# Performance work log

Measured on AMD Instinct MI355X. Metric: run time of the kernel, lower is better.

The kernel has to match this reference:

```python
import jax, jax.numpy as jnp
import numpy as np

EPS = 1e-5

def _bn(x, gamma, beta):
    # BatchNorm with track_running_stats=False: batch stats over all dims but last
    axes = tuple(range(x.ndim - 1))
    mu = jnp.mean(x, axis=axes)
    var = jnp.var(x, axis=axes)  # biased, as torch uses for normalization
    return (x - mu) * jax.lax.rsqrt(var + EPS) * gamma + beta

def setup_inputs() -> dict:
    B, N, D = 8, 200, 128
    key = jax.random.key(0)
    ks = jax.random.split(key, 14)
    s = 1.0 / np.sqrt(D)
    def w(k):
        return jax.random.uniform(k, (D, D), jnp.float32, -s, s)
    def b(k):
        return jax.random.uniform(k, (D,), jnp.float32, -s, s)
    return {
        'h': jax.random.normal(ks[0], (B, N, D), jnp.float32),
        'e': jax.random.normal(ks[1], (B, N, N, D), jnp.float32),
        'Uw': w(ks[2]), 'Ub': b(ks[3]),
        'Vw': w(ks[4]), 'Vb': b(ks[5]),
        'Aw': w(ks[6]), 'Ab': b(ks[7]),
        'Bw': w(ks[8]), 'Bb': b(ks[9]),
        'Cw': w(ks[10]), 'Cb': b(ks[11]),
        'gamma_h': jnp.ones((D,), jnp.float32), 'beta_h': jnp.zeros((D,), jnp.float32),
        'gamma_e': jnp.ones((D,), jnp.float32), 'beta_e': jnp.zeros((D,), jnp.float32),
    }

def reference(h, e, Uw, Ub, Vw, Vb, Aw, Ab, Bw, Bb, Cw, Cb,
              gamma_h, beta_h, gamma_e, beta_e):
    h_in, e_in = h, e
    Uh = h @ Uw.T + Ub                      # [B,N,D]
    Vh = h @ Vw.T + Vb                      # [B,N,D]
    Ah = h @ Aw.T + Ab
    Bh = h @ Bw.T + Bb
    Ce = e @ Cw.T + Cb                      # [B,N,N,D]
    # e_new[b,i,j,d] = Ah[b,j,d] + Bh[b,i,d] + Ce[b,i,j,d]
    e_new = Ah[:, None, :, :] + Bh[:, :, None, :] + Ce
    gates = jax.nn.sigmoid(e_new)           # [B,N,N,D]
    # sum aggregation over source nodes j with Vh broadcast over i
    agg = jnp.sum(gates * Vh[:, None, :, :], axis=2)  # [B,N,D]
    h_new = Uh + agg
    h_out = h_in + jax.nn.relu(_bn(h_new, gamma_h, beta_h))
    e_out = e_in + jax.nn.relu(_bn(e_new, gamma_e, beta_e))
    return (h_out, e_out)
```

## Files before the change

kernel.cpp:

```cpp
#include <hip/hip_runtime.h>
#include <hip/hip_bf16.h>


#define B_ 8
#define N_ 200
#define D_ 128
#define BN_ (B_*N_)
#define HN_ (BN_*D_)

typedef __attribute__((ext_vector_type(8))) short short8v;
typedef __attribute__((ext_vector_type(4))) short short4v;
typedef __attribute__((ext_vector_type(4))) float float4v;
typedef __attribute__((ext_vector_type(4))) unsigned int uint4v;

__device__ __forceinline__ unsigned short f2b(float f) {
  unsigned u = __float_as_uint(f);
  u += 0x7FFFu + ((u >> 16) & 1u);
  return (unsigned short)(u >> 16);
}

__global__ __launch_bounds__(256) void prelin_kernel(
    const float* __restrict__ h,
    const float* __restrict__ Uw, const float* __restrict__ Ub,
    const float* __restrict__ Vw, const float* __restrict__ Vb,
    const float* __restrict__ Aw, const float* __restrict__ Ab,
    const float* __restrict__ Bw, const float* __restrict__ Bb,
    const float* __restrict__ Cw,
    float* __restrict__ Uh, float* __restrict__ Vh,
    float* __restrict__ Ah, float* __restrict__ Bh,
    unsigned short* __restrict__ Cwbf) {
  const int tid = threadIdx.x;
  if (blockIdx.x >= 100) {
    int g = (blockIdx.x - 100) * 1024 + tid * 4;
    float4v v = *(const float4v*)(Cw + g);
    short4v s;
    s.x = (short)f2b(v.x); s.y = (short)f2b(v.y);
    s.z = (short)f2b(v.z); s.w = (short)f2b(v.w);
    *(short4v*)(Cwbf + g) = s;
    return;
  }
  const int r0 = blockIdx.x * 16;
  __shared__ float hs[16][128];
  for (int k = 0; k < 2; k++) {
    int g = k * 256 + tid;
    int row = g >> 5, col4 = g & 31;
    *(float4v*)&hs[row][col4 * 4] =
        *(const float4v*)(h + (size_t)(r0 + row) * D_ + col4 * 4);
  }
  __syncthreads();
  const int c0 = tid, c1 = tid + 256;
  const float* w0 = (c0 < 128) ? (Uw + c0 * 128) : (Vw + (c0 - 128) * 128);
  const float  b0 = (c0 < 128) ? Ub[c0] : Vb[c0 - 128];
  const float* w1 = (c1 < 384) ? (Aw + (c1 - 256) * 128) : (Bw + (c1 - 384) * 128);
  const float  b1 = (c1 < 384) ? Ab[c1 - 256] : Bb[c1 - 384];
  float acc0[16], acc1[16];
#pragma unroll
  for (int r = 0; r < 16; r++) { acc0[r] = 0.f; acc1[r] = 0.f; }
  for (int k = 0; k < 128; k += 4) {
    float4v w0v = *(const float4v*)(w0 + k);
    float4v w1v = *(const float4v*)(w1 + k);
#pragma unroll
    for (int r = 0; r < 16; r++) {
      float4v hv = *(const float4v*)&hs[r][k];
      acc0[r] = fmaf(hv.x, w0v.x, fmaf(hv.y, w0v.y, fmaf(hv.z, w0v.z, fmaf(hv.w, w0v.w, acc0[r]))));
      acc1[r] = fmaf(hv.x, w1v.x, fmaf(hv.y, w1v.y, fmaf(hv.z, w1v.z, fmaf(hv.w, w1v.w, acc1[r]))));
    }
  }
  float* dst0 = (c0 < 128) ? Uh : Vh; const int cc0 = c0 & 127;
  float* dst1 = (c1 < 384) ? Ah : Bh; const int cc1 = (c1 - 256) & 127;
#pragma unroll
  for (int r = 0; r < 16; r++) {
    dst0[(size_t)(r0 + r) * D_ + cc0] = acc0[r] + b0;
    dst1[(size_t)(r0 + r) * D_ + cc1] = acc1[r] + b1;
  }
}

template <int MODE>
__global__ __launch_bounds__(256, 2) void gemm_pass(
    const float* __restrict__ e, const unsigned short* __restrict__ Cwbf,
    const float* __restrict__ Cb, const float* __restrict__ Ah,
    const float* __restrict__ Bh, const float* __restrict__ Vh,
    float* __restrict__ agg, float* __restrict__ psum, float* __restrict__ psumsq,
    const float* __restrict__ scale_e, const float* __restrict__ shift_e,
    float* __restrict__ e_out) {
  const int tid = threadIdx.x;
  const int blk = blockIdx.x;
  const int b = blk / N_;
  const int lane = tid & 63, wz = tid >> 6;
  const int c = lane & 15, q = lane >> 4;

  __shared__ __align__(16) unsigned short Bs[128 * 136];
  __shared__ float base_s[128];
  __shared__ float ss_s[256];

  const uint4v* bsrc = (const uint4v*)Cwbf;
#pragma unroll
  for (int k2 = 0; k2 < 8; k2++) {
    int g = k2 * 256 + tid;
    int row = g >> 4, col = (g & 15) * 8;
    *(uint4v*)&Bs[row * 136 + col] = bsrc[g];
  }
  if (tid < 128) {
    base_s[tid] = Cb[tid] + Bh[(size_t)blk * D_ + tid];
    if (MODE == 1) { ss_s[tid] = scale_e[tid]; ss_s[128 + tid] = shift_e[tid]; }
  }
  __syncthreads();

  const float* erow = e + (size_t)blk * N_ * D_;
  const float* AhB = Ah + (size_t)b * N_ * D_;
  const float* VhB = (MODE == 0) ? (Vh + (size_t)b * N_ * D_) : nullptr;

  float aggv[8], sumv[8], sqv[8];
  if (MODE == 0) {
#pragma unroll
    for (int t = 0; t < 8; t++) { aggv[t] = 0.f; sumv[t] = 0.f; sqv[t] = 0.f; }
  }

  float4v ef[8];
  {
    const int j = wz * 16 + c;
    const float* p = erow + (size_t)j * D_ + q * 8;
    const bool ok = (j < N_);
#pragma unroll
    for (int l = 0; l < 4; l++) {
      ef[2 * l]     = ok ? *(const float4v*)(p + l * 32)     : (float4v){0.f,0.f,0.f,0.f};
      ef[2 * l + 1] = ok ? *(const float4v*)(p + l * 32 + 4) : (float4v){0.f,0.f,0.f,0.f};
    }
  }

#pragma unroll
  for (int jt = 0; jt < 4; jt++) {
    const int j0 = jt * 64;
    short8v av[4];
#pragma unroll
    for (int l = 0; l < 4; l++) {
      float4v v0 = ef[2 * l], v1 = ef[2 * l + 1];
      short8v s;
      s[0] = (short)f2b(v0.x); s[1] = (short)f2b(v0.y);
      s[2] = (short)f2b(v0.z); s[3] = (short)f2b(v0.w);
      s[4] = (short)f2b(v1.x); s[5] = (short)f2b(v1.y);
      s[6] = (short)f2b(v1.z); s[7] = (short)f2b(v1.w);
      av[l] = s;
    }
    if (jt < 3) {
      const int j = (jt + 1) * 64 + wz * 16 + c;
      const float* p = erow + (size_t)j * D_ + q * 8;
      const bool ok = (j < N_);
#pragma unroll
      for (int l = 0; l < 4; l++) {
        ef[2 * l]     = ok ? *(const float4v*)(p + l * 32)     : (float4v){0.f,0.f,0.f,0.f};
        ef[2 * l + 1] = ok ? *(const float4v*)(p + l * 32 + 4) : (float4v){0.f,0.f,0.f,0.f};
      }
    }

    float4v acc[8];
#pragma unroll
    for (int t = 0; t < 8; t++) acc[t] = (float4v){0.f, 0.f, 0.f, 0.f};
#pragma unroll
    for (int t = 0; t < 8; t++) {
      const unsigned short* brow = &Bs[(t * 16 + c) * 136 + q * 8];
#pragma unroll
      for (int l = 0; l < 4; l++) {
        short8v cw = *(const short8v*)(brow + l * 32);
        if (MODE == 0)
          acc[t] = __builtin_amdgcn_mfma_f32_16x16x32_bf16(av[l], cw, acc[t], 0, 0, 0);
        else
          acc[t] = __builtin_amdgcn_mfma_f32_16x16x32_bf16(cw, av[l], acc[t], 0, 0, 0);
      }
    }

    if (MODE == 0) {
#pragma unroll
      for (int t = 0; t < 8; t++) {
        const int n = t * 16 + c;
        const float bse = base_s[n];
#pragma unroll
        for (int r = 0; r < 4; r++) {
          const int j = j0 + wz * 16 + q * 4 + r;
          if (j < N_) {
            float x = acc[t][r] + bse + AhB[(size_t)j * D_ + n];
            float g = __builtin_amdgcn_rcpf(1.0f + __expf(-x));
            aggv[t] += g * VhB[(size_t)j * D_ + n];
            sumv[t] += x;
            sqv[t] += x * x;
          }
        }
      }
    } else {
      const int j = j0 + wz * 16 + c;
      if (j < N_) {
        const size_t rowoff = (size_t)blk * N_ * D_ + (size_t)j * D_;
#pragma unroll
        for (int t = 0; t < 8; t++) {
          const int n4 = t * 16 + q * 4;
          float4v ah = *(const float4v*)(AhB + (size_t)j * D_ + n4);
          float4v bs4 = *(const float4v*)&base_s[n4];
          float4v sc4 = *(const float4v*)&ss_s[n4];
          float4v sh4 = *(const float4v*)&ss_s[128 + n4];
          float4v ein = *(const float4v*)(e + rowoff + n4);
          float4v o;
#pragma unroll
          for (int r = 0; r < 4; r++) {
            float x = acc[t][r] + bs4[r] + ah[r];
            float y = fmaxf(x * sc4[r] + sh4[r], 0.f);
            o[r] = ein[r] + y;
          }
          *(float4v*)(e_out + rowoff + n4) = o;
        }
      }
    }
  }

  if (MODE == 0) {
    __syncthreads();
    float* red = (float*)Bs;
#pragma unroll
    for (int t = 0; t < 8; t++) {
      float a = aggv[t], s = sumv[t], sq2 = sqv[t];
      a += __shfl_xor(a, 16); a += __shfl_xor(a, 32);
      s += __shfl_xor(s, 16); s += __shfl_xor(s, 32);
      sq2 += __shfl_xor(sq2, 16); sq2 += __shfl_xor(sq2, 32);
      if (q == 0) {
        red[(0 * 4 + wz) * 128 + t * 16 + c] = a;
        red[(1 * 4 + wz) * 128 + t * 16 + c] = s;
        red[(2 * 4 + wz) * 128 + t * 16 + c] = sq2;
      }
    }
    __syncthreads();
    if (tid < 128) {
      float a = 0.f, s = 0.f, sq2 = 0.f;
#pragma unroll
      for (int w = 0; w < 4; w++) {
        a += red[(0 * 4 + w) * 128 + tid];
        s += red[(1 * 4 + w) * 128 + tid];
        sq2 += red[(2 * 4 + w) * 128 + tid];
      }
      agg[(size_t)blk * D_ + tid] = a;
      psum[(size_t)blk * D_ + tid] = s;
      psumsq[(size_t)blk * D_ + tid] = sq2;
    }
  }
}

__global__ __launch_bounds__(256) void stats_part(
    const float* __restrict__ psum, const float* __restrict__ psumsq,
    const float* __restrict__ Uh, const float* __restrict__ agg,
    float* __restrict__ partial) {
  const int t = threadIdx.x, blk = blockIdx.x;
  const int cg = t & 31, rs = t >> 5;
  float4v ps = {0,0,0,0}, pq = {0,0,0,0}, hs = {0,0,0,0}, hq = {0,0,0,0};
#pragma unroll
  for (int p = 0; p < 2; p++) {
    const int row = blk * 16 + p * 8 + rs;
    const size_t off = (size_t)row * D_ + cg * 4;
    float4v a = *(const float4v*)(psum + off);
    float4v bq = *(const float4v*)(psumsq + off);
    float4v u = *(const float4v*)(Uh + off);
    float4v g = *(const float4v*)(agg + off);
    ps += a; pq += bq;
    float4v hv = u + g;
    hs += hv; hq += hv * hv;
  }
  __shared__ float4v red[4][8][32];
  red[0][rs][cg] = ps; red[1][rs][cg] = pq; red[2][rs][cg] = hs; red[3][rs][cg] = hq;
  __syncthreads();
  if (t < 128) {
    const int s = t >> 5, g = t & 31;
    float4v acc = red[s][0][g];
#pragma unroll
    for (int r = 1; r < 8; r++) acc += red[s][r][g];
    *(float4v*)(partial + (size_t)blk * 512 + s * 128 + g * 4) = acc;
  }
}

__global__ __launch_bounds__(128) void stats_final(
    const float* __restrict__ partial,
    const float* __restrict__ gamma_h, const float* __restrict__ beta_h,
    const float* __restrict__ gamma_e, const float* __restrict__ beta_e,
    float* __restrict__ scale_e, float* __restrict__ shift_e,
    float* __restrict__ scale_h, float* __restrict__ shift_h) {
  const int n = threadIdx.x;
  float s = 0.f, sq = 0.f, hs = 0.f, hq = 0.f;
  for (int p = 0; p < 100; p++) {
    const float* base = partial + (size_t)p * 512;
    s += base[n]; sq += base[128 + n]; hs += base[256 + n]; hq += base[384 + n];
  }
  const float Me = 8.f * 200.f * 200.f;
  float mean = s / Me;
  float var = sq / Me - mean * mean;
  float sce = gamma_e[n] * rsqrtf(var + 1e-5f);
  scale_e[n] = sce; shift_e[n] = beta_e[n] - mean * sce;
  const float Mh = (float)BN_;
  float mh = hs / Mh;
  float vh = hq / Mh - mh * mh;
  float sch = gamma_h[n] * rsqrtf(vh + 1e-5f);
  scale_h[n] = sch; shift_h[n] = beta_h[n] - mh * sch;
}

__global__ __launch_bounds__(256) void hpath_kernel(
    const float* __restrict__ h, const float* __restrict__ Uh,
    const float* __restrict__ agg, const float* __restrict__ scale_h,
    const float* __restrict__ shift_h, float* __restrict__ h_out) {
  const int idx = blockIdx.x * 256 + threadIdx.x;
  float4v u = ((const float4v*)Uh)[idx];
  float4v a = ((const float4v*)agg)[idx];
  float4v hv = ((const float4v*)h)[idx];
  float4v sc = ((const float4v*)scale_h)[idx & 31];
  float4v sh = ((const float4v*)shift_h)[idx & 31];
  float4v o;
#pragma unroll
  for (int l = 0; l < 4; l++) {
    float y = fmaxf((u[l] + a[l]) * sc[l] + sh[l], 0.f);
    o[l] = hv[l] + y;
  }
  ((float4v*)h_out)[idx] = o;
}

extern "C" void kernel_launch(void* const* d_in, const int* in_sizes, int n_in,
                              void* d_out, int out_size, void* d_ws, size_t ws_size,
                              hipStream_t stream) {
  const float* h  = (const float*)d_in[0];
  const float* e  = (const float*)d_in[1];
  const float* Uw = (const float*)d_in[2];  const float* Ub = (const float*)d_in[3];
  const float* Vw = (const float*)d_in[4];  const float* Vb = (const float*)d_in[5];
  const float* Aw = (const float*)d_in[6];  const float* Ab = (const float*)d_in[7];
  const float* Bw = (const float*)d_in[8];  const float* Bb = (const float*)d_in[9];
  const float* Cw = (const float*)d_in[10]; const float* Cb = (const float*)d_in[11];
  const float* gamma_h = (const float*)d_in[12]; const float* beta_h = (const float*)d_in[13];
  const float* gamma_e = (const float*)d_in[14]; const float* beta_e = (const float*)d_in[15];

  float* ws = (float*)d_ws;
  float* Uh = ws + 0;
  float* Vh = ws + (size_t)HN_;
  float* Ah = ws + (size_t)HN_ * 2;
  float* Bh = ws + (size_t)HN_ * 3;
  float* agg = ws + (size_t)HN_ * 4;
  float* psum = ws + (size_t)HN_ * 5;
  float* psumsq = ws + (size_t)HN_ * 6;
  float* scale_e = ws + (size_t)HN_ * 7;
  float* shift_e = scale_e + 128;
  float* scale_h = scale_e + 256;
  float* shift_h = scale_e + 384;
  unsigned short* Cwbf = (unsigned short*)(scale_e + 512);
  float* partial = scale_e + 512 + 8192;

  float* h_out = (float*)d_out;
  float* e_out = (float*)d_out + HN_;

  prelin_kernel<<<116, 256, 0, stream>>>(h, Uw, Ub, Vw, Vb, Aw, Ab, Bw, Bb, Cw,
                                         Uh, Vh, Ah, Bh, Cwbf);
  gemm_pass<0><<<BN_, 256, 0, stream>>>(e, Cwbf, Cb, Ah, Bh, Vh,
                                        agg, psum, psumsq,
                                        nullptr, nullptr, nullptr);
  stats_part<<<100, 256, 0, stream>>>(psum, psumsq, Uh, agg, partial);
  stats_final<<<1, 128, 0, stream>>>(partial, gamma_h, beta_h, gamma_e, beta_e,
                                     scale_e, shift_e, scale_h, shift_h);
  hpath_kernel<<<200, 256, 0, stream>>>(h, Uh, agg, scale_h, shift_h, h_out);
  gemm_pass<1><<<BN_, 256, 0, stream>>>(e, Cwbf, Cb, Ah, Bh, nullptr,
                                        nullptr, nullptr, nullptr,
                                        scale_e, shift_e, e_out);
}
```

Baseline: 487.3 us.

## Transpose Ah/Vh, swizzle LDS weights, fuse h-path into second pass, raise occupancy

```diff
diff --git a/kernel.cpp b/kernel.cpp
--- a/kernel.cpp
+++ b/kernel.cpp
@@ -1,5 +1,4 @@
 #include <hip/hip_runtime.h>
-#include <hip/hip_bf16.h>
 
 
 #define B_ 8
@@ -17,6 +16,16 @@
   unsigned u = __float_as_uint(f);
   u += 0x7FFFu + ((u >> 16) & 1u);
   return (unsigned short)(u >> 16);
+}
+
+__device__ __forceinline__ short8v cvt_bf16x8(float4v lo, float4v hi) {
+  unsigned int r0, r1, r2, r3;
+  asm("v_cvt_pk_bf16_f32 %0, %1, %2" : "=v"(r0) : "v"(lo.x), "v"(lo.y));
+  asm("v_cvt_pk_bf16_f32 %0, %1, %2" : "=v"(r1) : "v"(lo.z), "v"(lo.w));
+  asm("v_cvt_pk_bf16_f32 %0, %1, %2" : "=v"(r2) : "v"(hi.x), "v"(hi.y));
+  asm("v_cvt_pk_bf16_f32 %0, %1, %2" : "=v"(r3) : "v"(hi.z), "v"(hi.w));
+  uint4v u; u.x = r0; u.y = r1; u.z = r2; u.w = r3;
+  return __builtin_bit_cast(short8v, u);
 }
 
 __global__ __launch_bounds__(256) void prelin_kernel(
@@ -25,9 +34,10 @@
     const float* __restrict__ Vw, const float* __restrict__ Vb,
     const float* __restrict__ Aw, const float* __restrict__ Ab,
     const float* __restrict__ Bw, const float* __restrict__ Bb,
-    const float* __restrict__ Cw,
-    float* __restrict__ Uh, float* __restrict__ Vh,
-    float* __restrict__ Ah, float* __restrict__ Bh,
+    const float* __restrict__ Cw, const float* __restrict__ Cb,
+    float* __restrict__ Uh, float* __restrict__ VhT,
+    float* __restrict__ Ah, float* __restrict__ AhT,
+    float* __restrict__ BhC,
     unsigned short* __restrict__ Cwbf) {
   const int tid = threadIdx.x;
   if (blockIdx.x >= 100) {
@@ -52,7 +62,7 @@
   const float* w0 = (c0 < 128) ? (Uw + c0 * 128) : (Vw + (c0 - 128) * 128);
   const float  b0 = (c0 < 128) ? Ub[c0] : Vb[c0 - 128];
   const float* w1 = (c1 < 384) ? (Aw + (c1 - 256) * 128) : (Bw + (c1 - 384) * 128);
-  const float  b1 = (c1 < 384) ? Ab[c1 - 256] : Bb[c1 - 384];
+  const float  b1 = (c1 < 384) ? Ab[c1 - 256] : (Bb[c1 - 384] + Cb[c1 - 384]);
   float acc0[16], acc1[16];
 #pragma unroll
   for (int r = 0; r < 16; r++) { acc0[r] = 0.f; acc1[r] = 0.f; }
@@ -66,55 +76,92 @@
       acc1[r] = fmaf(hv.x, w1v.x, fmaf(hv.y, w1v.y, fmaf(hv.z, w1v.z, fmaf(hv.w, w1v.w, acc1[r]))));
     }
   }
-  float* dst0 = (c0 < 128) ? Uh : Vh; const int cc0 = c0 & 127;
-  float* dst1 = (c1 < 384) ? Ah : Bh; const int cc1 = (c1 - 256) & 127;
+  const int cc0 = c0 & 127;
+  const int cc1 = (c1 - 256) & 127;
 #pragma unroll
   for (int r = 0; r < 16; r++) {
-    dst0[(size_t)(r0 + r) * D_ + cc0] = acc0[r] + b0;
-    dst1[(size_t)(r0 + r) * D_ + cc1] = acc1[r] + b1;
+    const int g = r0 + r;
+    const int bb = g / 200;
+    const int ii = g - bb * 200;
+    float v0 = acc0[r] + b0;
+    if (c0 < 128) Uh[(size_t)g * D_ + cc0] = v0;
+    else          VhT[((size_t)bb * D_ + cc0) * N_ + ii] = v0;
+    float v1 = acc1[r] + b1;
+    if (c1 < 384) {
+      Ah[(size_t)g * D_ + cc1] = v1;
+      AhT[((size_t)bb * D_ + cc1) * N_ + ii] = v1;
+    } else {
+      BhC[(size_t)g * D_ + cc1] = v1;
+    }
   }
 }
 
 template <int MODE>
-__global__ __launch_bounds__(256, 2) void gemm_pass(
+__global__ __launch_bounds__(256, 5) void gemm_pass(
     const float* __restrict__ e, const unsigned short* __restrict__ Cwbf,
-    const float* __restrict__ Cb, const float* __restrict__ Ah,
-    const float* __restrict__ Bh, const float* __restrict__ Vh,
+    const float* __restrict__ BhC, const float* __restrict__ Ah,
+    const float* __restrict__ AhT, const float* __restrict__ VhT,
     float* __restrict__ agg, float* __restrict__ psum, float* __restrict__ psumsq,
     const float* __restrict__ scale_e, const float* __restrict__ shift_e,
-    float* __restrict__ e_out) {
+    float* __restrict__ e_out,
+    const float* __restrict__ hin, const float* __restrict__ Uh,
+    const float* __restrict__ scale_h, const float* __restrict__ shift_h,
+    float* __restrict__ h_out) {
   const int tid = threadIdx.x;
+
+  if (MODE == 1 && blockIdx.x >= BN_) {
+    const int idx = (blockIdx.x - BN_) * 256 + tid;
+    float4v u = ((const float4v*)Uh)[idx];
+    float4v a = ((const float4v*)agg)[idx];
+    float4v hv = ((const float4v*)hin)[idx];
+    float4v sc = ((const float4v*)scale_h)[idx & 31];
+    float4v sh = ((const float4v*)shift_h)[idx & 31];
+    float4v o;
+#pragma unroll
+    for (int l = 0; l < 4; l++) {
+      float y = fmaxf(fmaf(u[l] + a[l], sc[l], sh[l]), 0.f);
+      o[l] = hv[l] + y;
+    }
+    ((float4v*)h_out)[idx] = o;
+    return;
+  }
+
   const int blk = blockIdx.x;
   const int b = blk / N_;
   const int lane = tid & 63, wz = tid >> 6;
   const int c = lane & 15, q = lane >> 4;
 
-  __shared__ __align__(16) unsigned short Bs[128 * 136];
-  __shared__ float base_s[128];
-  __shared__ float ss_s[256];
+  __shared__ __align__(16) unsigned short Bs[128 * 128];
 
   const uint4v* bsrc = (const uint4v*)Cwbf;
 #pragma unroll
   for (int k2 = 0; k2 < 8; k2++) {
     int g = k2 * 256 + tid;
-    int row = g >> 4, col = (g & 15) * 8;
-    *(uint4v*)&Bs[row * 136 + col] = bsrc[g];
-  }
-  if (tid < 128) {
-    base_s[tid] = Cb[tid] + Bh[(size_t)blk * D_ + tid];
-    if (MODE == 1) { ss_s[tid] = scale_e[tid]; ss_s[128 + tid] = shift_e[tid]; }
+    int row = g >> 4;
+    int col16 = (g & 15) ^ (row & 7);
+    *(uint4v*)&Bs[row * 128 + col16 * 8] = bsrc[g];
+  }
+
+  float bsev[8];
+  if (MODE == 0) {
+#pragma unroll
+    for (int t = 0; t < 8; t++) bsev[t] = BhC[(size_t)blk * D_ + t * 16 + c];
   }
   __syncthreads();
 
   const float* erow = e + (size_t)blk * N_ * D_;
   const float* AhB = Ah + (size_t)b * N_ * D_;
-  const float* VhB = (MODE == 0) ? (Vh + (size_t)b * N_ * D_) : nullptr;
+  const float* AhTb = AhT + (size_t)b * D_ * N_;
+  const float* VhTb = VhT + (size_t)b * D_ * N_;
+  const float* BhCrow = BhC + (size_t)blk * D_;
 
   float aggv[8], sumv[8], sqv[8];
   if (MODE == 0) {
 #pragma unroll
     for (int t = 0; t < 8; t++) { aggv[t] = 0.f; sumv[t] = 0.f; sqv[t] = 0.f; }
   }
+
+  const int sw = c & 7;
 
   float4v ef[8];
   {
@@ -133,15 +180,8 @@
     const int j0 = jt * 64;
     short8v av[4];
 #pragma unroll
-    for (int l = 0; l < 4; l++) {
-      float4v v0 = ef[2 * l], v1 = ef[2 * l + 1];
-      short8v s;
-      s[0] = (short)f2b(v0.x); s[1] = (short)f2b(v0.y);
-      s[2] = (short)f2b(v0.z); s[3] = (short)f2b(v0.w);
-      s[4] = (short)f2b(v1.x); s[5] = (short)f2b(v1.y);
-      s[6] = (short)f2b(v1.z); s[7] = (short)f2b(v1.w);
-      av[l] = s;
-    }
+    for (int l = 0; l < 4; l++) av[l] = cvt_bf16x8(ef[2 * l], ef[2 * l + 1]);
+
     if (jt < 3) {
       const int j = (jt + 1) * 64 + wz * 16 + c;
       const float* p = erow + (size_t)j * D_ + q * 8;
@@ -158,10 +198,10 @@
     for (int t = 0; t < 8; t++) acc[t] = (float4v){0.f, 0.f, 0.f, 0.f};
 #pragma unroll
     for (int t = 0; t < 8; t++) {
-      const unsigned short* brow = &Bs[(t * 16 + c) * 136 + q * 8];
+      const unsigned short* brow = &Bs[(t * 16 + c) * 128];
 #pragma unroll
       for (int l = 0; l < 4; l++) {
-        short8v cw = *(const short8v*)(brow + l * 32);
+        short8v cw = *(const short8v*)(brow + (((q | (l << 2)) ^ sw) << 3));
         if (MODE == 0)
           acc[t] = __builtin_amdgcn_mfma_f32_16x16x32_bf16(av[l], cw, acc[t], 0, 0, 0);
         else
@@ -170,20 +210,25 @@
     }
 
     if (MODE == 0) {
-#pragma unroll
-      for (int t = 0; t < 8; t++) {
-        const int n = t * 16 + c;
-        const float bse = base_s[n];
-#pragma unroll
-        for (int r = 0; r < 4; r++) {
-          const int j = j0 + wz * 16 + q * 4 + r;
-          if (j < N_) {
-            float x = acc[t][r] + bse + AhB[(size_t)j * D_ + n];
+      const int jb = j0 + wz * 16 + q * 4;
+      if (jb < N_) {
+        const float* pA = AhTb + (size_t)c * N_ + jb;
+        const float* pV = VhTb + (size_t)c * N_ + jb;
+#pragma unroll
+        for (int t = 0; t < 8; t++) {
+          float4v ah4 = *(const float4v*)(pA + (size_t)t * 16 * N_);
+          float4v vh4 = *(const float4v*)(pV + (size_t)t * 16 * N_);
+          const float bse = bsev[t];
+          float ag = aggv[t], sm = sumv[t], sq2 = sqv[t];
+#pragma unroll
+          for (int r = 0; r < 4; r++) {
+            float x = acc[t][r] + bse + ah4[r];
             float g = __builtin_amdgcn_rcpf(1.0f + __expf(-x));
-            aggv[t] += g * VhB[(size_t)j * D_ + n];
-            sumv[t] += x;
-            sqv[t] += x * x;
+            ag = fmaf(g, vh4[r], ag);
+            sm += x;
+            sq2 = fmaf(x, x, sq2);
           }
+          aggv[t] = ag; sumv[t] = sm; sqv[t] = sq2;
         }
       }
     } else {
@@ -194,15 +239,15 @@
         for (int t = 0; t < 8; t++) {
           const int n4 = t * 16 + q * 4;
           float4v ah = *(const float4v*)(AhB + (size_t)j * D_ + n4);
-          float4v bs4 = *(const float4v*)&base_s[n4];
-          float4v sc4 = *(const float4v*)&ss_s[n4];
-          float4v sh4 = *(const float4v*)&ss_s[128 + n4];
+          float4v bs4 = *(const float4v*)(BhCrow + n4);
+          float4v sc4 = *(const float4v*)(scale_e + n4);
+          float4v sh4 = *(const float4v*)(shift_e + n4);
           float4v ein = *(const float4v*)(e + rowoff + n4);
           float4v o;
 #pragma unroll
           for (int r = 0; r < 4; r++) {
             float x = acc[t][r] + bs4[r] + ah[r];
-            float y = fmaxf(x * sc4[r] + sh4[r], 0.f);
+            float y = fmaxf(fmaf(x, sc4[r], sh4[r]), 0.f);
             o[r] = ein[r] + y;
           }
           *(float4v*)(e_out + rowoff + n4) = o;
@@ -273,47 +318,37 @@
   }
 }
 
-__global__ __launch_bounds__(128) void stats_final(
+__global__ __launch_bounds__(256) void stats_final(
     const float* __restrict__ partial,
     const float* __restrict__ gamma_h, const float* __restrict__ beta_h,
     const float* __restrict__ gamma_e, const float* __restrict__ beta_e,
     float* __restrict__ scale_e, float* __restrict__ shift_e,
     float* __restrict__ scale_h, float* __restrict__ shift_h) {
-  const int n = threadIdx.x;
-  float s = 0.f, sq = 0.f, hs = 0.f, hq = 0.f;
-  for (int p = 0; p < 100; p++) {
-    const float* base = partial + (size_t)p * 512;
-    s += base[n]; sq += base[128 + n]; hs += base[256 + n]; hq += base[384 + n];
-  }
-  const float Me = 8.f * 200.f * 200.f;
-  float mean = s / Me;
-  float var = sq / Me - mean * mean;
-  float sce = gamma_e[n] * rsqrtf(var + 1e-5f);
-  scale_e[n] = sce; shift_e[n] = beta_e[n] - mean * sce;
-  const float Mh = (float)BN_;
-  float mh = hs / Mh;
-  float vh = hq / Mh - mh * mh;
-  float sch = gamma_h[n] * rsqrtf(vh + 1e-5f);
-  scale_h[n] = sch; shift_h[n] = beta_h[n] - mh * sch;
-}
-
-__global__ __launch_bounds__(256) void hpath_kernel(
-    const float* __restrict__ h, const float* __restrict__ Uh,
-    const float* __restrict__ agg, const float* __restrict__ scale_h,
-    const float* __restrict__ shift_h, float* __restrict__ h_out) {
-  const int idx = blockIdx.x * 256 + threadIdx.x;
-  float4v u = ((const float4v*)Uh)[idx];
-  float4v a = ((const float4v*)agg)[idx];
-  float4v hv = ((const float4v*)h)[idx];
-  float4v sc = ((const float4v*)scale_h)[idx & 31];
-  float4v sh = ((const float4v*)shift_h)[idx & 31];
-  float4v o;
-#pragma unroll
-  for (int l = 0; l < 4; l++) {
-    float y = fmaxf((u[l] + a[l]) * sc[l] + sh[l], 0.f);
-    o[l] = hv[l] + y;
-  }
-  ((float4v*)h_out)[idx] = o;
+  const int t = threadIdx.x;
+  const int n = t & 127;
+  if (t < 128) {
+    float s = 0.f, sq = 0.f;
+    for (int p = 0; p < 100; p++) {
+      const float* base = partial + (size_t)p * 512;
+      s += base[n]; sq += base[128 + n];
+    }
+    const float Me = 8.f * 200.f * 200.f;
+    float mean = s / Me;
+    float var = sq / Me - mean * mean;
+    float sce = gamma_e[n] * rsqrtf(var + 1e-5f);
+    scale_e[n] = sce; shift_e[n] = beta_e[n] - mean * sce;
+  } else {
+    float hs = 0.f, hq = 0.f;
+    for (int p = 0; p < 100; p++) {
+      const float* base = partial + (size_t)p * 512;
+      hs += base[256 + n]; hq += base[384 + n];
+    }
+    const float Mh = (float)BN_;
+    float mh = hs / Mh;
+    float vh = hq / Mh - mh * mh;
+    float sch = gamma_h[n] * rsqrtf(vh + 1e-5f);
+    scale_h[n] = sch; shift_h[n] = beta_h[n] - mh * sch;
+  }
 }
 
 extern "C" void kernel_launch(void* const* d_in, const int* in_sizes, int n_in,
@@ -330,14 +365,15 @@
   const float* gamma_e = (const float*)d_in[14]; const float* beta_e = (const float*)d_in[15];
 
   float* ws = (float*)d_ws;
-  float* Uh = ws + 0;
-  float* Vh = ws + (size_t)HN_;
-  float* Ah = ws + (size_t)HN_ * 2;
-  float* Bh = ws + (size_t)HN_ * 3;
-  float* agg = ws + (size_t)HN_ * 4;
+  float* Uh   = ws + 0;
+  float* VhT  = ws + (size_t)HN_;
+  float* Ah   = ws + (size_t)HN_ * 2;
+  float* BhC  = ws + (size_t)HN_ * 3;
+  float* agg  = ws + (size_t)HN_ * 4;
   float* psum = ws + (size_t)HN_ * 5;
   float* psumsq = ws + (size_t)HN_ * 6;
-  float* scale_e = ws + (size_t)HN_ * 7;
+  float* AhT  = ws + (size_t)HN_ * 7;
+  float* scale_e = ws + (size_t)HN_ * 8;
   float* shift_e = scale_e + 128;
   float* scale_h = scale_e + 256;
   float* shift_h = scale_e + 384;
@@ -347,16 +383,17 @@
   float* h_out = (float*)d_out;
   float* e_out = (float*)d_out + HN_;
 
-  prelin_kernel<<<116, 256, 0, stream>>>(h, Uw, Ub, Vw, Vb, Aw, Ab, Bw, Bb, Cw,
-                                         Uh, Vh, Ah, Bh, Cwbf);
-  gemm_pass<0><<<BN_, 256, 0, stream>>>(e, Cwbf, Cb, Ah, Bh, Vh,
+  prelin_kernel<<<116, 256, 0, stream>>>(h, Uw, Ub, Vw, Vb, Aw, Ab, Bw, Bb, Cw, Cb,
+                                         Uh, VhT, Ah, AhT, BhC, Cwbf);
+  gemm_pass<0><<<BN_, 256, 0, stream>>>(e, Cwbf, BhC, Ah, AhT, VhT,
                                         agg, psum, psumsq,
-                                        nullptr, nullptr, nullptr);
+                                        nullptr, nullptr, nullptr,
+                                        nullptr, nullptr, nullptr, nullptr, nullptr);
   stats_part<<<100, 256, 0, stream>>>(psum, psumsq, Uh, agg, partial);
-  stats_final<<<1, 128, 0, stream>>>(partial, gamma_h, beta_h, gamma_e, beta_e,
+  stats_final<<<1, 256, 0, stream>>>(partial, gamma_h, beta_h, gamma_e, beta_e,
                                      scale_e, shift_e, scale_h, shift_h);
-  hpath_kernel<<<200, 256, 0, stream>>>(h, Uh, agg, scale_h, shift_h, h_out);
-  gemm_pass<1><<<BN_, 256, 0, stream>>>(e, Cwbf, Cb, Ah, Bh, nullptr,
-                                        nullptr, nullptr, nullptr,
-                                        scale_e, shift_e, e_out);
-}
+  gemm_pass<1><<<BN_ + 200, 256, 0, stream>>>(e, Cwbf, BhC, Ah, AhT, VhT,
+                                              agg, psum, psumsq,
+                                              scale_e, shift_e, e_out,
+                                              h, Uh, scale_h, shift_h, h_out);
+}
```

Measured after the change: 605.2 us. 24.2% more time.
